# Performance work log

Hardware: AMD Instinct MI355X
Metric: run time of the kernel (lower is better)

The kernel has to match this reference:

```python
import jax, jax.numpy as jnp
import numpy as np

NUM_HEADS = 4
GROUPS = 16
EPS = 1e-5


def setup_inputs() -> dict:
    key = jax.random.key(0)
    ks = jax.random.split(key, 7)
    b, c, hh, ww = 4, 256, 64, 64
    x = jax.random.normal(ks[0], (b, c, hh, ww), dtype=jnp.float32)
    norm_w = 1.0 + 0.1 * jax.random.normal(ks[1], (c,), dtype=jnp.float32)
    norm_b = 0.1 * jax.random.normal(ks[2], (c,), dtype=jnp.float32)
    qkv_w = jax.random.normal(ks[3], (3 * c, c), dtype=jnp.float32) / np.sqrt(c)
    qkv_b = 0.01 * jax.random.normal(ks[4], (3 * c,), dtype=jnp.float32)
    # NOTE: original zero-inits proj_out; we use random weights so the
    # attention path actually affects the output (kernel correctness test).
    proj_w = jax.random.normal(ks[5], (c, c), dtype=jnp.float32) / np.sqrt(c)
    proj_b = jnp.zeros((c,), dtype=jnp.float32)
    return {"x": x, "norm_w": norm_w, "norm_b": norm_b,
            "qkv_w": qkv_w, "qkv_b": qkv_b,
            "proj_w": proj_w, "proj_b": proj_b}


def _group_norm(x, w, b):
    # x: [B, C, T]; GroupNorm32 computes in fp32 (inputs already fp32)
    B, C, T = x.shape
    xg = x.reshape(B, GROUPS, C // GROUPS, T)
    mean = jnp.mean(xg, axis=(2, 3), keepdims=True)
    var = jnp.var(xg, axis=(2, 3), keepdims=True)
    xn = ((xg - mean) * jax.lax.rsqrt(var + EPS)).reshape(B, C, T)
    return xn * w[None, :, None] + b[None, :, None]


def reference(x, norm_w, norm_b, qkv_w, qkv_b, proj_w, proj_b):
    b, c = x.shape[0], x.shape[1]
    spatial = x.shape[2:]
    x2 = x.reshape(b, c, -1)                       # [B, C, T]
    T = x2.shape[-1]
    normed = _group_norm(x2, norm_w, norm_b)
    qkv = jnp.einsum('oc,bct->bot', qkv_w, normed) + qkv_b[None, :, None]
    # faithful reshape: [B, 3C, T] -> [B*H, 3C/H, T], then split in thirds
    qkv = qkv.reshape(b * NUM_HEADS, (3 * c) // NUM_HEADS, T)
    ch = qkv.shape[1] // 3                         # = C / H
    q, k, v = jnp.split(qkv, 3, axis=1)
    scale = 1.0 / np.sqrt(np.sqrt(ch))
    weight = jnp.einsum('bct,bcs->bts', q * scale, k * scale)
    weight = jax.nn.softmax(weight.astype(jnp.float32), axis=-1).astype(qkv.dtype)
    h = jnp.einsum('bts,bcs->bct', weight, v)      # [B*H, ch, T]
    h = h.reshape(b, c, T)
    h = jnp.einsum('oc,bct->bot', proj_w, h) + proj_b[None, :, None]
    return (x2 + h).reshape(b, c, *spatial)
```

## Files before the change

### kernel.cpp

```cpp
#include <hip/hip_runtime.h>

constexpr int kB  = 4;
constexpr int kC  = 256;
constexpr int kT  = 4096;
constexpr int kG  = 16;
constexpr int kCg = kC / kG;
constexpr int kH  = 4;
constexpr int kCh = kC / kH;
constexpr float kEps = 1e-5f;
constexpr float kQScale = 0.125f * 1.4426950408889634f;

typedef short bf16x8 __attribute__((ext_vector_type(8)));
typedef float f32x4  __attribute__((ext_vector_type(4)));
typedef float f32x16 __attribute__((ext_vector_type(16)));

__device__ inline unsigned short f2bf(float f) {
    union { float f; unsigned u; } v; v.f = f;
    unsigned r = v.u + 0x7fffu + ((v.u >> 16) & 1u);
    return (unsigned short)(r >> 16);
}
__device__ inline unsigned pk2bf(float a, float b) {
    return (unsigned)f2bf(a) | ((unsigned)f2bf(b) << 16);
}
__device__ inline unsigned pk2bf_trunc(float a, float b) {
    return __builtin_amdgcn_perm(__float_as_uint(b), __float_as_uint(a), 0x07060302u);
}
__device__ inline void pls32(unsigned& a, unsigned& b) {
    __asm__("v_permlane32_swap_b32 %0, %1" : "+v"(a), "+v"(b));
}

__global__ __launch_bounds__(256) void prep_kernel(const float* __restrict__ x,
                                                   float* __restrict__ stats,
                                                   const float* __restrict__ qkv_w,
                                                   const float* __restrict__ proj_w,
                                                   unsigned short* __restrict__ wbf) {
    int tid = threadIdx.x;
    if (blockIdx.x >= 64) {
        int gid = (blockIdx.x - 64) * 256 + tid;
        for (int i = gid; i < 65536; i += 128 * 256) {
            float4 v = (i < 49152) ? ((const float4*)qkv_w)[i]
                                   : ((const float4*)proj_w)[i - 49152];
            *(uint2*)&wbf[(size_t)i * 4] = make_uint2(pk2bf(v.x, v.y), pk2bf(v.z, v.w));
        }
        return;
    }
    int bg = blockIdx.x;
    const float4* xp4 = (const float4*)(x + (size_t)bg * (kCg * kT));
    float s = 0.f, q = 0.f;
    #pragma unroll 4
    for (int i = 0; i < (kCg * kT / 4) / 256; ++i) {
        float4 v = xp4[tid + i * 256];
        s += v.x + v.y + v.z + v.w;
        q += v.x * v.x + v.y * v.y + v.z * v.z + v.w * v.w;
    }
    #pragma unroll
    for (int off = 32; off > 0; off >>= 1) {
        s += __shfl_down(s, off);
        q += __shfl_down(q, off);
    }
    __shared__ float rs[4], rq[4];
    int wid = tid >> 6, lane = tid & 63;
    if (lane == 0) { rs[wid] = s; rq[wid] = q; }
    __syncthreads();
    if (tid == 0) {
        float S = rs[0] + rs[1] + rs[2] + rs[3];
        float Q = rq[0] + rq[1] + rq[2] + rq[3];
        const float invN = 1.0f / (float)(kCg * kT);
        float mean = S * invN;
        float var  = Q * invN - mean * mean;
        stats[bg * 2 + 0] = mean;
        stats[bg * 2 + 1] = rsqrtf(var + kEps);
    }
}

__global__ __launch_bounds__(256) void gn_apply_t_kernel(const float* __restrict__ x,
                                                         const float* __restrict__ stats,
                                                         const float* __restrict__ w,
                                                         const float* __restrict__ bias,
                                                         unsigned short* __restrict__ normT) {
    __shared__ float Ls[64][65];
    int t0 = blockIdx.x * 64;
    int c0 = blockIdx.y * 64;
    int b  = blockIdx.z;
    int tid = threadIdx.x;
    #pragma unroll
    for (int p = 0; p < 4; ++p) {
        int idx = tid + p * 256;
        int cl = idx >> 4, t4 = idx & 15;
        int c = c0 + cl;
        int bg = b * kG + (c >> 4);
        float mean = stats[bg * 2 + 0];
        float rstd = stats[bg * 2 + 1];
        float sw = w[c] * rstd;
        float sb = bias[c] - mean * sw;
        float4 v = *(const float4*)&x[((size_t)b * kC + c) * kT + t0 + t4 * 4];
        Ls[t4 * 4 + 0][cl] = v.x * sw + sb;
        Ls[t4 * 4 + 1][cl] = v.y * sw + sb;
        Ls[t4 * 4 + 2][cl] = v.z * sw + sb;
        Ls[t4 * 4 + 3][cl] = v.w * sw + sb;
    }
    __syncthreads();
    {
        int row = tid >> 2, cq = (tid & 3) * 16;
        unsigned tmp[8];
        #pragma unroll
        for (int i = 0; i < 8; ++i)
            tmp[i] = pk2bf(Ls[row][cq + 2 * i], Ls[row][cq + 2 * i + 1]);
        uint4* dst = (uint4*)&normT[((size_t)b * kT + t0 + row) * kC + c0 + cq];
        dst[0] = make_uint4(tmp[0], tmp[1], tmp[2], tmp[3]);
        dst[1] = make_uint4(tmp[4], tmp[5], tmp[6], tmp[7]);
    }
}

__global__ __launch_bounds__(256) void qkv_gemm_kernel(const unsigned short* __restrict__ wbf,
                                                       const float* __restrict__ qkv_b,
                                                       const unsigned short* __restrict__ normT,
                                                       unsigned short* __restrict__ qTg,
                                                       unsigned short* __restrict__ kTg,
                                                       unsigned short* __restrict__ vCg) {
    constexpr int LDK = 72;
    constexpr int LDV = 136;
    __shared__ __align__(16) unsigned short As[64 * LDK];
    __shared__ __align__(16) unsigned short Bs[128 * LDK];

    int t0 = blockIdx.x * 128;
    int m0 = blockIdx.y * 64;
    int b  = blockIdx.z;
    const unsigned short* Ab = wbf + (size_t)m0 * kC;
    const unsigned short* Bb = normT + (size_t)b * kT * kC;

    int tid = threadIdx.x;
    int wave = tid >> 6, lane = tid & 63;
    int ln15 = lane & 15, quad = lane >> 4;
    int wm = wave >> 1, wt = wave & 1;

    f32x4 acc[2][4] = {};

    for (int k0 = 0; k0 < kC; k0 += 64) {
        __syncthreads();
        #pragma unroll
        for (int p = 0; p < 2; ++p) {
            int idx = tid + p * 256;
            int row = idx >> 3, seg = idx & 7;
            *(uint4*)&As[row * LDK + seg * 8] =
                *(const uint4*)&Ab[(size_t)row * kC + k0 + seg * 8];
        }
        #pragma unroll
        for (int p = 0; p < 4; ++p) {
            int idx = tid + p * 256;
            int row = idx >> 3, seg = idx & 7;
            *(uint4*)&Bs[row * LDK + seg * 8] =
                *(const uint4*)&Bb[(size_t)(t0 + row) * kC + k0 + seg * 8];
        }
        __syncthreads();
        #pragma unroll
        for (int ks = 0; ks < 2; ++ks) {
            bf16x8 af[2], bf[4];
            #pragma unroll
            for (int i = 0; i < 2; ++i)
                af[i] = *(bf16x8*)&As[(wm * 32 + i * 16 + ln15) * LDK + ks * 32 + quad * 8];
            #pragma unroll
            for (int j = 0; j < 4; ++j)
                bf[j] = *(bf16x8*)&Bs[(wt * 64 + j * 16 + ln15) * LDK + ks * 32 + quad * 8];
            #pragma unroll
            for (int i = 0; i < 2; ++i)
                #pragma unroll
                for (int j = 0; j < 4; ++j)
                    acc[i][j] = __builtin_amdgcn_mfma_f32_16x16x32_bf16(
                        af[i], bf[j], acc[i][j], 0, 0, 0);
        }
    }

    int type = (m0 % 192) / 64;
    int h = m0 / 192;
    int bh = b * kH + h;
    __syncthreads();
    #pragma unroll
    for (int i = 0; i < 2; ++i) {
        float4 bv = *(const float4*)&qkv_b[m0 + wm * 32 + i * 16 + quad * 4];
        const float* bp = (const float*)&bv;
        #pragma unroll
        for (int j = 0; j < 4; ++j) {
            int tl = wt * 64 + j * 16 + ln15;
            int c = wm * 32 + i * 16 + quad * 4;
            float v0 = acc[i][j][0] + bp[0];
            float v1 = acc[i][j][1] + bp[1];
            float v2 = acc[i][j][2] + bp[2];
            float v3 = acc[i][j][3] + bp[3];
            if (type == 0) {
                v0 *= kQScale; v1 *= kQScale; v2 *= kQScale; v3 *= kQScale;
            }
            if (type != 2) {
                *(uint2*)&Bs[tl * LDK + c] = make_uint2(pk2bf(v0, v1), pk2bf(v2, v3));
            } else {
                Bs[(c + 0) * LDV + tl] = f2bf(v0);
                Bs[(c + 1) * LDV + tl] = f2bf(v1);
                Bs[(c + 2) * LDV + tl] = f2bf(v2);
                Bs[(c + 3) * LDV + tl] = f2bf(v3);
            }
        }
    }
    __syncthreads();
    if (type != 2) {
        unsigned short* base = ((type == 0) ? qTg : kTg) + (size_t)bh * (kT * kCh);
        #pragma unroll
        for (int p = 0; p < 4; ++p) {
            int f = tid + p * 256;
            int ln = f & 31, hif = (f >> 5) & 1, ks = (f >> 6) & 3, tb = f >> 8;
            *(uint4*)&base[((t0 >> 5) + tb) * 2048 + ks * 512 + hif * 256 + ln * 8] =
                *(uint4*)&Bs[(tb * 32 + ln) * LDK + ks * 16 + hif * 8];
        }
    } else {
        unsigned short* base = vCg + (size_t)bh * (kT * kCh);
        #pragma unroll
        for (int p = 0; p < 4; ++p) {
            int f = tid + p * 256;
            int c = f & 63, hif = (f >> 6) & 1, sg = f >> 7;
            *(uint4*)&base[((t0 >> 4) + sg) * 1024 + hif * 512 + c * 8] =
                *(uint4*)&Bs[c * LDV + sg * 16 + hif * 8];
        }
    }
}

__global__ __launch_bounds__(256, 2) void attn_mfma_kernel(const unsigned short* __restrict__ qTg,
                                                           const unsigned short* __restrict__ kTg,
                                                           const unsigned short* __restrict__ vCg,
                                                           unsigned short* __restrict__ attnT) {
    __shared__ float Ored[2][2][32][64];
    __shared__ float Lred[2][2][64];

    int lid = blockIdx.y * 32 + blockIdx.x;
    int wl  = (lid & 7) * 64 + (lid >> 3);
    int bh  = wl >> 5;
    int t0  = (wl & 31) * 128;
    int b = bh >> 2, h = bh & 3;

    int tid = threadIdx.x;
    int wave = tid >> 6, lane = tid & 63;
    int ln31 = lane & 31, hi = lane >> 5;
    int tc = wave & 1;
    int sh = wave >> 1;

    const unsigned short* qb = qTg + (size_t)bh * (kT * kCh);
    const unsigned short* kb = kTg + (size_t)bh * (kT * kCh);
    const unsigned short* vb = vCg + (size_t)bh * (kT * kCh);

    bf16x8 qA[4], qB[4];
    {
        const unsigned short* qp = qb + ((size_t)(t0 >> 5) + tc * 2) * 2048 + hi * 256 + ln31 * 8;
        #pragma unroll
        for (int ks = 0; ks < 4; ++ks) {
            qA[ks] = *(const bf16x8*)(qp + ks * 512);
            qB[ks] = *(const bf16x8*)(qp + 2048 + ks * 512);
        }
    }

    const unsigned short* kbase = kb + (size_t)sh * 131072 + hi * 256 + ln31 * 8;
    const unsigned short* vbase = vb + (size_t)sh * 131072 + hi * 512 + ln31 * 8;

    float lA = 0.f, lB = 0.f;
    f32x16 oA0 = {}, oA1 = {}, oB0 = {}, oB1 = {};
    union PunP { uint4 u; bf16x8 f; };

    auto loadKV = [&](bf16x8* kf, bf16x8* vf, int idx) {
        const unsigned short* kp = kbase + (size_t)idx * 2048;
        const unsigned short* vp = vbase + (size_t)idx * 2048;
        kf[0] = *(const bf16x8*)(kp);
        kf[1] = *(const bf16x8*)(kp + 512);
        kf[2] = *(const bf16x8*)(kp + 1024);
        kf[3] = *(const bf16x8*)(kp + 1536);
        vf[0] = *(const bf16x8*)(vp);
        vf[1] = *(const bf16x8*)(vp + 256);
        vf[2] = *(const bf16x8*)(vp + 1024);
        vf[3] = *(const bf16x8*)(vp + 1280);
    };

    auto softmax_pack = [&](const f32x16& s, float& l, bf16x8& f0, bf16x8& f1) {
        unsigned u00, u01, u10, u11, u20, u21, u30, u31;
        {
            float p0 = __builtin_amdgcn_exp2f(s[0]);
            float p1 = __builtin_amdgcn_exp2f(s[1]);
            float p2 = __builtin_amdgcn_exp2f(s[2]);
            float p3 = __builtin_amdgcn_exp2f(s[3]);
            l += (p0 + p1) + (p2 + p3);
            u00 = pk2bf_trunc(p0, p1); u01 = pk2bf_trunc(p2, p3);
        }
        {
            float p0 = __builtin_amdgcn_exp2f(s[4]);
            float p1 = __builtin_amdgcn_exp2f(s[5]);
            float p2 = __builtin_amdgcn_exp2f(s[6]);
            float p3 = __builtin_amdgcn_exp2f(s[7]);
            l += (p0 + p1) + (p2 + p3);
            u10 = pk2bf_trunc(p0, p1); u11 = pk2bf_trunc(p2, p3);
        }
        {
            float p0 = __builtin_amdgcn_exp2f(s[8]);
            float p1 = __builtin_amdgcn_exp2f(s[9]);
            float p2 = __builtin_amdgcn_exp2f(s[10]);
            float p3 = __builtin_amdgcn_exp2f(s[11]);
            l += (p0 + p1) + (p2 + p3);
            u20 = pk2bf_trunc(p0, p1); u21 = pk2bf_trunc(p2, p3);
        }
        {
            float p0 = __builtin_amdgcn_exp2f(s[12]);
            float p1 = __builtin_amdgcn_exp2f(s[13]);
            float p2 = __builtin_amdgcn_exp2f(s[14]);
            float p3 = __builtin_amdgcn_exp2f(s[15]);
            l += (p0 + p1) + (p2 + p3);
            u30 = pk2bf_trunc(p0, p1); u31 = pk2bf_trunc(p2, p3);
        }
        pls32(u00, u10); pls32(u01, u11);
        pls32(u20, u30); pls32(u21, u31);
        PunP P0, P1;
        P0.u = make_uint4(u00, u01, u10, u11);
        P1.u = make_uint4(u20, u21, u30, u31);
        f0 = P0.f; f1 = P1.f;
    };

    auto computeTile = [&](const bf16x8* kf, const bf16x8* vf) {
        f32x16 sA = {}, sB = {};
        __builtin_amdgcn_s_setprio(1);
        #pragma unroll
        for (int ks = 0; ks < 4; ++ks) {
            sA = __builtin_amdgcn_mfma_f32_32x32x16_bf16(kf[ks], qA[ks], sA, 0, 0, 0);
            sB = __builtin_amdgcn_mfma_f32_32x32x16_bf16(kf[ks], qB[ks], sB, 0, 0, 0);
        }
        __builtin_amdgcn_s_setprio(0);
        bf16x8 FA0, FA1, FB0, FB1;
        softmax_pack(sA, lA, FA0, FA1);
        softmax_pack(sB, lB, FB0, FB1);
        __builtin_amdgcn_s_setprio(1);
        oA0 = __builtin_amdgcn_mfma_f32_32x32x16_bf16(vf[0], FA0, oA0, 0, 0, 0);
        oA1 = __builtin_amdgcn_mfma_f32_32x32x16_bf16(vf[1], FA0, oA1, 0, 0, 0);
        oB0 = __builtin_amdgcn_mfma_f32_32x32x16_bf16(vf[0], FB0, oB0, 0, 0, 0);
        oB1 = __builtin_amdgcn_mfma_f32_32x32x16_bf16(vf[1], FB0, oB1, 0, 0, 0);
        oA0 = __builtin_amdgcn_mfma_f32_32x32x16_bf16(vf[2], FA1, oA0, 0, 0, 0);
        oA1 = __builtin_amdgcn_mfma_f32_32x32x16_bf16(vf[3], FA1, oA1, 0, 0, 0);
        oB0 = __builtin_amdgcn_mfma_f32_32x32x16_bf16(vf[2], FB1, oB0, 0, 0, 0);
        oB1 = __builtin_amdgcn_mfma_f32_32x32x16_bf16(vf[3], FB1, oB1, 0, 0, 0);
        __builtin_amdgcn_s_setprio(0);
    };

    bf16x8 kX[4], vX[4], kY[4], vY[4];
    loadKV(kX, vX, 0);
    #pragma unroll 1
    for (int it = 0; it < 64; it += 2) {
        loadKV(kY, vY, it + 1);
        computeTile(kX, vX);
        loadKV(kX, vX, (it + 2) & 63);
        computeTile(kY, vY);
    }

    lA += __shfl_xor(lA, 32);
    lB += __shfl_xor(lB, 32);

    if (sh == 1) {
        #pragma unroll
        for (int e = 0; e < 16; ++e) {
            Ored[tc][0][e][lane]      = oA0[e];
            Ored[tc][0][16 + e][lane] = oA1[e];
            Ored[tc][1][e][lane]      = oB0[e];
            Ored[tc][1][16 + e][lane] = oB1[e];
        }
        Lred[tc][0][lane] = lA;
        Lred[tc][1][lane] = lB;
    }
    __syncthreads();
    if (sh == 0) {
        #pragma unroll
        for (int e = 0; e < 16; ++e) {
            oA0[e] += Ored[tc][0][e][lane];
            oA1[e] += Ored[tc][0][16 + e][lane];
            oB0[e] += Ored[tc][1][e][lane];
            oB1[e] += Ored[tc][1][16 + e][lane];
        }
        lA += Lred[tc][0][lane];
        lB += Lred[tc][1][lane];
        #pragma unroll
        for (int ch = 0; ch < 2; ++ch) {
            float linv = 1.0f / (ch ? lB : lA);
            int t = t0 + tc * 64 + ch * 32 + ln31;
            #pragma unroll
            for (int ct = 0; ct < 2; ++ct) {
                const f32x16& ao = ch ? (ct ? oB1 : oB0) : (ct ? oA1 : oA0);
                #pragma unroll
                for (int g = 0; g < 4; ++g) {
                    int c = h * kCh + ct * 32 + 8 * g + 4 * hi;
                    float v0 = ao[4 * g + 0] * linv;
                    float v1 = ao[4 * g + 1] * linv;
                    float v2 = ao[4 * g + 2] * linv;
                    float v3 = ao[4 * g + 3] * linv;
                    *(uint2*)&attnT[((size_t)b * kT + t) * kC + c] =
                        make_uint2(pk2bf(v0, v1), pk2bf(v2, v3));
                }
            }
        }
    }
}

__global__ __launch_bounds__(256) void proj_gemm_kernel(const unsigned short* __restrict__ wpbf,
                                                        const float* __restrict__ proj_b,
                                                        const unsigned short* __restrict__ attnT,
                                                        const float* __restrict__ x,
                                                        float* __restrict__ out) {
    constexpr int LDK = 72;
    __shared__ __align__(16) unsigned short As[64 * LDK];
    __shared__ __align__(16) unsigned short Bs[128 * LDK];

    int t0 = blockIdx.x * 128;
    int m0 = blockIdx.y * 64;
    int b  = blockIdx.z;
    const unsigned short* Ab = wpbf + (size_t)m0 * kC;
    const unsigned short* Bb = attnT + (size_t)b * kT * kC;

    int tid = threadIdx.x;
    int wave = tid >> 6, lane = tid & 63;
    int ln15 = lane & 15, quad = lane >> 4;
    int wm = wave >> 1, wt = wave & 1;

    f32x4 acc[2][4] = {};

    for (int k0 = 0; k0 < kC; k0 += 64) {
        __syncthreads();
        #pragma unroll
        for (int p = 0; p < 2; ++p) {
            int idx = tid + p * 256;
            int row = idx >> 3, seg = idx & 7;
            *(uint4*)&As[row * LDK + seg * 8] =
                *(const uint4*)&Ab[(size_t)row * kC + k0 + seg * 8];
        }
        #pragma unroll
        for (int p = 0; p < 4; ++p) {
            int idx = tid + p * 256;
            int row = idx >> 3, seg = idx & 7;
            *(uint4*)&Bs[row * LDK + seg * 8] =
                *(const uint4*)&Bb[(size_t)(t0 + row) * kC + k0 + seg * 8];
        }
        __syncthreads();
        #pragma unroll
        for (int ks = 0; ks < 2; ++ks) {
            bf16x8 af[2], bf[4];
            #pragma unroll
            for (int i = 0; i < 2; ++i)
                af[i] = *(bf16x8*)&As[(wm * 32 + i * 16 + ln15) * LDK + ks * 32 + quad * 8];
            #pragma unroll
            for (int j = 0; j < 4; ++j)
                bf[j] = *(bf16x8*)&Bs[(wt * 64 + j * 16 + ln15) * LDK + ks * 32 + quad * 8];
            #pragma unroll
            for (int i = 0; i < 2; ++i)
                #pragma unroll
                for (int j = 0; j < 4; ++j)
                    acc[i][j] = __builtin_amdgcn_mfma_f32_16x16x32_bf16(
                        af[i], bf[j], acc[i][j], 0, 0, 0);
        }
    }

    #pragma unroll
    for (int i = 0; i < 2; ++i) {
        float4 bv = *(const float4*)&proj_b[m0 + wm * 32 + i * 16 + quad * 4];
        const float* bp = (const float*)&bv;
        #pragma unroll
        for (int j = 0; j < 4; ++j) {
            int t = t0 + wt * 64 + j * 16 + ln15;
            int mbase = m0 + wm * 32 + i * 16 + quad * 4;
            #pragma unroll
            for (int r = 0; r < 4; ++r) {
                size_t off = ((size_t)b * kC + mbase + r) * kT + t;
                out[off] = acc[i][j][r] + bp[r] + x[off];
            }
        }
    }
}

extern "C" void kernel_launch(void* const* d_in, const int* in_sizes, int n_in,
                              void* d_out, int out_size, void* d_ws, size_t ws_size,
                              hipStream_t stream) {
    const float* x      = (const float*)d_in[0];
    const float* norm_w = (const float*)d_in[1];
    const float* norm_b = (const float*)d_in[2];
    const float* qkv_w  = (const float*)d_in[3];
    const float* qkv_b  = (const float*)d_in[4];
    const float* proj_w = (const float*)d_in[5];
    const float* proj_b = (const float*)d_in[6];
    float* out = (float*)d_out;

    float* stats = (float*)d_ws;
    unsigned short* wsbf  = (unsigned short*)((float*)d_ws + 128);
    unsigned short* normT = wsbf;
    unsigned short* wbf   = normT + (size_t)kB * kT * kC;
    unsigned short* qTp   = wbf + 262144;
    unsigned short* kTp   = qTp + (size_t)kB * kH * kT * kCh;
    unsigned short* vCp   = kTp + (size_t)kB * kH * kT * kCh;
    unsigned short* attnT = vCp + (size_t)kB * kH * kT * kCh;
    unsigned short* wpbf  = wbf + 196608;

    prep_kernel<<<192, 256, 0, stream>>>(x, stats, qkv_w, proj_w, wbf);
    gn_apply_t_kernel<<<dim3(kT / 64, kC / 64, kB), 256, 0, stream>>>(
        x, stats, norm_w, norm_b, normT);
    qkv_gemm_kernel<<<dim3(kT / 128, 12, kB), 256, 0, stream>>>(
        wbf, qkv_b, normT, qTp, kTp, vCp);
    attn_mfma_kernel<<<dim3(kT / 128, kB * kH), 256, 0, stream>>>(qTp, kTp, vCp, attnT);
    proj_gemm_kernel<<<dim3(kT / 128, kC / 64, kB), 256, 0, stream>>>(
        wpbf, proj_b, attnT, x, out);
}
```

Measured before the change: 195.7 us.

## Stage K/V tiles through LDS with async global_load_lds ring buffer

Replaces per-wave direct global loads of K and V fragments, where both tc waves loaded the same data, with a 4-deep LDS ring filled by global_load_lds. Each wave issues one quarter of the tile copy, and waits use vmcnt plus a barrier. This removes duplicate global traffic and register-held double buffers, and overlaps prefetch three tiles ahead. The cost is a block barrier every iteration and LDS reads, and the reduction buffers are aliased onto the K/V LDS storage.

Result: slower. 202.8 us (+3.6%).

```diff
diff --git a/kernel.cpp b/kernel.cpp
--- a/kernel.cpp
+++ b/kernel.cpp
@@ -27,6 +27,11 @@
 }
 __device__ inline void pls32(unsigned& a, unsigned& b) {
     __asm__("v_permlane32_swap_b32 %0, %1" : "+v"(a), "+v"(b));
+}
+__device__ inline void llds16(const unsigned short* g, unsigned short* l) {
+    __builtin_amdgcn_global_load_lds(
+        (const __attribute__((address_space(1))) unsigned int*)(g),
+        (__attribute__((address_space(3))) unsigned int*)(l), 16, 0, 0);
 }
 
 __global__ __launch_bounds__(256) void prep_kernel(const float* __restrict__ x,
@@ -226,8 +231,7 @@
                                                            const unsigned short* __restrict__ kTg,
                                                            const unsigned short* __restrict__ vCg,
                                                            unsigned short* __restrict__ attnT) {
-    __shared__ float Ored[2][2][32][64];
-    __shared__ float Lred[2][2][64];
+    __shared__ __align__(16) unsigned short kvS[4][2][2][2048];
 
     int lid = blockIdx.y * 32 + blockIdx.x;
     int wl  = (lid & 7) * 64 + (lid >> 3);
@@ -255,25 +259,21 @@
         }
     }
 
-    const unsigned short* kbase = kb + (size_t)sh * 131072 + hi * 256 + ln31 * 8;
-    const unsigned short* vbase = vb + (size_t)sh * 131072 + hi * 512 + ln31 * 8;
+    const unsigned short* gsrc = ((wave & 1) ? vb : kb)
+                               + (size_t)(wave >> 1) * 131072 + lane * 8;
+    unsigned short* lbase = &kvS[0][wave >> 1][wave & 1][0];
+
+    auto fill = [&](int buf, int tile) {
+        const unsigned short* s = gsrc + (size_t)tile * 2048;
+        unsigned short* d = lbase + buf * 8192;
+        #pragma unroll
+        for (int j = 0; j < 4; ++j)
+            llds16(s + j * 512, d + j * 512);
+    };
 
     float lA = 0.f, lB = 0.f;
     f32x16 oA0 = {}, oA1 = {}, oB0 = {}, oB1 = {};
     union PunP { uint4 u; bf16x8 f; };
-
-    auto loadKV = [&](bf16x8* kf, bf16x8* vf, int idx) {
-        const unsigned short* kp = kbase + (size_t)idx * 2048;
-        const unsigned short* vp = vbase + (size_t)idx * 2048;
-        kf[0] = *(const bf16x8*)(kp);
-        kf[1] = *(const bf16x8*)(kp + 512);
-        kf[2] = *(const bf16x8*)(kp + 1024);
-        kf[3] = *(const bf16x8*)(kp + 1536);
-        vf[0] = *(const bf16x8*)(vp);
-        vf[1] = *(const bf16x8*)(vp + 256);
-        vf[2] = *(const bf16x8*)(vp + 1024);
-        vf[3] = *(const bf16x8*)(vp + 1280);
-    };
 
     auto softmax_pack = [&](const f32x16& s, float& l, bf16x8& f0, bf16x8& f1) {
         unsigned u00, u01, u10, u11, u20, u21, u30, u31;
@@ -317,7 +317,27 @@
         f0 = P0.f; f1 = P1.f;
     };
 
-    auto computeTile = [&](const bf16x8* kf, const bf16x8* vf) {
+    fill(0, 0); fill(1, 1); fill(2, 2);
+
+    #pragma unroll 1
+    for (int it = 0; it < 64; ++it) {
+        if (it <= 61)      __asm__ __volatile__("s_waitcnt vmcnt(8)" ::: "memory");
+        else if (it == 62) __asm__ __volatile__("s_waitcnt vmcnt(4)" ::: "memory");
+        else               __asm__ __volatile__("s_waitcnt vmcnt(0)" ::: "memory");
+        __builtin_amdgcn_s_barrier();
+        if (it <= 60) fill((it + 3) & 3, it + 3);
+
+        const unsigned short* Kh = &kvS[it & 3][sh][0][0];
+        const unsigned short* Vh = &kvS[it & 3][sh][1][0];
+        bf16x8 kf[4], vf[4];
+        #pragma unroll
+        for (int ks = 0; ks < 4; ++ks)
+            kf[ks] = *(const bf16x8*)&Kh[ks * 512 + hi * 256 + ln31 * 8];
+        vf[0] = *(const bf16x8*)&Vh[0    + hi * 512 + ln31 * 8];
+        vf[1] = *(const bf16x8*)&Vh[256  + hi * 512 + ln31 * 8];
+        vf[2] = *(const bf16x8*)&Vh[1024 + hi * 512 + ln31 * 8];
+        vf[3] = *(const bf16x8*)&Vh[1280 + hi * 512 + ln31 * 8];
+
         f32x16 sA = {}, sB = {};
         __builtin_amdgcn_s_setprio(1);
         #pragma unroll
@@ -339,43 +359,38 @@
         oB0 = __builtin_amdgcn_mfma_f32_32x32x16_bf16(vf[2], FB1, oB0, 0, 0, 0);
         oB1 = __builtin_amdgcn_mfma_f32_32x32x16_bf16(vf[3], FB1, oB1, 0, 0, 0);
         __builtin_amdgcn_s_setprio(0);
-    };
-
-    bf16x8 kX[4], vX[4], kY[4], vY[4];
-    loadKV(kX, vX, 0);
-    #pragma unroll 1
-    for (int it = 0; it < 64; it += 2) {
-        loadKV(kY, vY, it + 1);
-        computeTile(kX, vX);
-        loadKV(kX, vX, (it + 2) & 63);
-        computeTile(kY, vY);
     }
 
     lA += __shfl_xor(lA, 32);
     lB += __shfl_xor(lB, 32);
 
+    __asm__ __volatile__("" ::: "memory");
+    __builtin_amdgcn_s_barrier();
+    __asm__ __volatile__("" ::: "memory");
+    float* OredP = (float*)&kvS[0][0][0][0];
+    float* LredP = (float*)((char*)&kvS[0][0][0][0] + 32768);
     if (sh == 1) {
         #pragma unroll
         for (int e = 0; e < 16; ++e) {
-            Ored[tc][0][e][lane]      = oA0[e];
-            Ored[tc][0][16 + e][lane] = oA1[e];
-            Ored[tc][1][e][lane]      = oB0[e];
-            Ored[tc][1][16 + e][lane] = oB1[e];
-        }
-        Lred[tc][0][lane] = lA;
-        Lred[tc][1][lane] = lB;
+            OredP[((tc * 2 + 0) * 32 + e)      * 64 + lane] = oA0[e];
+            OredP[((tc * 2 + 0) * 32 + 16 + e) * 64 + lane] = oA1[e];
+            OredP[((tc * 2 + 1) * 32 + e)      * 64 + lane] = oB0[e];
+            OredP[((tc * 2 + 1) * 32 + 16 + e) * 64 + lane] = oB1[e];
+        }
+        LredP[(tc * 2 + 0) * 64 + lane] = lA;
+        LredP[(tc * 2 + 1) * 64 + lane] = lB;
     }
     __syncthreads();
     if (sh == 0) {
         #pragma unroll
         for (int e = 0; e < 16; ++e) {
-            oA0[e] += Ored[tc][0][e][lane];
-            oA1[e] += Ored[tc][0][16 + e][lane];
-            oB0[e] += Ored[tc][1][e][lane];
-            oB1[e] += Ored[tc][1][16 + e][lane];
-        }
-        lA += Lred[tc][0][lane];
-        lB += Lred[tc][1][lane];
+            oA0[e] += OredP[((tc * 2 + 0) * 32 + e)      * 64 + lane];
+            oA1[e] += OredP[((tc * 2 + 0) * 32 + 16 + e) * 64 + lane];
+            oB0[e] += OredP[((tc * 2 + 1) * 32 + e)      * 64 + lane];
+            oB1[e] += OredP[((tc * 2 + 1) * 32 + 16 + e) * 64 + lane];
+        }
+        lA += LredP[(tc * 2 + 0) * 64 + lane];
+        lB += LredP[(tc * 2 + 1) * 64 + lane];
         #pragma unroll
         for (int ch = 0; ch < 2; ++ch) {
             float linv = 1.0f / (ch ? lB : lA);
```

## Software-pipeline QK^T of next tile ahead of softmax and PV of current tile

Applied to the files above, without the earlier changes.

Splits the per-tile attention step into a score block (QK^T MFMAs) and a finish step (exp2 softmax pack plus PV MFMAs), and restructures the loop so the scores for tile n+1 are computed before the softmax of tile n. K and V loads are also separated and issued at different points. The intent is to let the exp2/pack VALU work overlap with independent MFMA work and hide load latency. The cost is extra live accumulator registers (two more f32x16 score sets), which may raise register pressure or lower occupancy.

New measurement: 200.0 us. 2.2% more time.

```diff
diff --git a/kernel.cpp b/kernel.cpp
--- a/kernel.cpp
+++ b/kernel.cpp
@@ -262,17 +262,31 @@
     f32x16 oA0 = {}, oA1 = {}, oB0 = {}, oB1 = {};
     union PunP { uint4 u; bf16x8 f; };
 
-    auto loadKV = [&](bf16x8* kf, bf16x8* vf, int idx) {
+    auto loadK = [&](bf16x8* kf, int idx) {
         const unsigned short* kp = kbase + (size_t)idx * 2048;
-        const unsigned short* vp = vbase + (size_t)idx * 2048;
         kf[0] = *(const bf16x8*)(kp);
         kf[1] = *(const bf16x8*)(kp + 512);
         kf[2] = *(const bf16x8*)(kp + 1024);
         kf[3] = *(const bf16x8*)(kp + 1536);
+    };
+    auto loadV = [&](bf16x8* vf, int idx) {
+        const unsigned short* vp = vbase + (size_t)idx * 2048;
         vf[0] = *(const bf16x8*)(vp);
         vf[1] = *(const bf16x8*)(vp + 256);
         vf[2] = *(const bf16x8*)(vp + 1024);
         vf[3] = *(const bf16x8*)(vp + 1280);
+    };
+
+    auto sBlock = [&](const bf16x8* kf, f32x16& sA, f32x16& sB) {
+        f32x16 a = {}, c = {};
+        __builtin_amdgcn_s_setprio(1);
+        #pragma unroll
+        for (int ks = 0; ks < 4; ++ks) {
+            a = __builtin_amdgcn_mfma_f32_32x32x16_bf16(kf[ks], qA[ks], a, 0, 0, 0);
+            c = __builtin_amdgcn_mfma_f32_32x32x16_bf16(kf[ks], qB[ks], c, 0, 0, 0);
+        }
+        __builtin_amdgcn_s_setprio(0);
+        sA = a; sB = c;
     };
 
     auto softmax_pack = [&](const f32x16& s, float& l, bf16x8& f0, bf16x8& f1) {
@@ -317,15 +331,7 @@
         f0 = P0.f; f1 = P1.f;
     };
 
-    auto computeTile = [&](const bf16x8* kf, const bf16x8* vf) {
-        f32x16 sA = {}, sB = {};
-        __builtin_amdgcn_s_setprio(1);
-        #pragma unroll
-        for (int ks = 0; ks < 4; ++ks) {
-            sA = __builtin_amdgcn_mfma_f32_32x32x16_bf16(kf[ks], qA[ks], sA, 0, 0, 0);
-            sB = __builtin_amdgcn_mfma_f32_32x32x16_bf16(kf[ks], qB[ks], sB, 0, 0, 0);
-        }
-        __builtin_amdgcn_s_setprio(0);
+    auto finishTile = [&](const f32x16& sA, const f32x16& sB, const bf16x8* vf) {
         bf16x8 FA0, FA1, FB0, FB1;
         softmax_pack(sA, lA, FA0, FA1);
         softmax_pack(sB, lB, FB0, FB1);
@@ -341,15 +347,29 @@
         __builtin_amdgcn_s_setprio(0);
     };
 
-    bf16x8 kX[4], vX[4], kY[4], vY[4];
-    loadKV(kX, vX, 0);
+    bf16x8 K0[4], V0[4], K1[4], V1[4];
+    f32x16 sCA, sCB, sNA, sNB;
+
+    loadK(K0, 0); loadV(V0, 0);
+    loadK(K1, 1); loadV(V1, 1);
+    sBlock(K0, sCA, sCB);
+
     #pragma unroll 1
-    for (int it = 0; it < 64; it += 2) {
-        loadKV(kY, vY, it + 1);
-        computeTile(kX, vX);
-        loadKV(kX, vX, (it + 2) & 63);
-        computeTile(kY, vY);
-    }
+    for (int it = 0; it < 62; it += 2) {
+        sBlock(K1, sNA, sNB);
+        loadK(K0, it + 2);
+        finishTile(sCA, sCB, V0);
+        loadV(V0, it + 2);
+        sCA = sNA; sCB = sNB;
+        sBlock(K0, sNA, sNB);
+        loadK(K1, it + 3);
+        finishTile(sCA, sCB, V1);
+        loadV(V1, it + 3);
+        sCA = sNA; sCB = sNB;
+    }
+    sBlock(K1, sNA, sNB);
+    finishTile(sCA, sCB, V0);
+    finishTile(sNA, sNB, V1);
 
     lA += __shfl_xor(lA, 32);
     lB += __shfl_xor(lB, 32);
```
